# Kernel optimization log

Measured on AMD Instinct MI355X. Metric: run time of the kernel, lower is better.

Reference implementation:

```python
import jax, jax.numpy as jnp
import numpy as np

H = W = 64
ALPHA = 1.0
BETA = 100.0
LIMB_PAIRS = np.array([[0,1],[1,2],[2,3],[0,4],[4,5],[5,6],[0,7],[7,8],[8,9],[9,10],
                       [8,11],[11,12],[12,13],[8,14],[14,15],[15,16]])
P0 = LIMB_PAIRS[:, 0]
P1 = LIMB_PAIRS[:, 1]
_last = {}
for _l, _j in enumerate(P0):
    _last[int(_j)] = _l
J0 = np.array(list(_last.keys()))   # unique proximal joints
L0 = np.array(list(_last.values())) # last limb writing to each joint


def make_kernel(h, w, alpha):
    # replicates: coords = stack(meshgrid(arange(2h-1), arange(2w-1))).transpose(1,2) (h==w)
    ii, jj = jnp.meshgrid(jnp.arange(2 * h - 1), jnp.arange(2 * w - 1), indexing='ij')
    ker = jnp.stack([h - jj, w - ii], axis=0).astype(jnp.float32)  # (2, 2h-1, 2w-1)
    dist = jnp.linalg.norm(ker, axis=0, keepdims=True)
    dist = dist.at[0, h, w].set(1.0)
    return ker / dist ** (1.0 + alpha)


def corr_full(x, k):
    # x: (N, Cin, h, w); k: (Cout, Cin, 2h-1, 2w-1); 'same' correlation with pad h-1/w-1
    h, w = x.shape[-2:]
    return jax.lax.conv_general_dilated(x, k, (1, 1), ((h - 1, h - 1), (w - 1, w - 1)))


def heatmap_std(x, di=False):
    axes = (3, 4, 5) if di else (3, 4)
    return jnp.std(x, axis=axes, keepdims=True, ddof=1)


def heatmap_normalize(x, std, di=False):
    return x * std / (heatmap_std(x, di) + 1e-6)


def l2norm(v, axis):
    return v / jnp.maximum(jnp.linalg.norm(v, axis=axis, keepdims=True), 1e-12)


def soft_argmax(hm, beta):
    # hm: ... x h x w -> ... x 2 with (row_coord, col_coord) as in the torch code
    h, w = hm.shape[-2:]
    p = jax.nn.softmax(hm.reshape(hm.shape[:-2] + (-1,)) * beta, axis=-1).reshape(hm.shape)
    rows = jnp.arange(h, dtype=p.dtype)[:, None]
    cols = jnp.arange(w, dtype=p.dtype)[None, :]
    norm = p.sum((-2, -1))
    kp_x = (p * rows).sum((-2, -1)) / norm
    kp_y = (p * cols).sum((-2, -1)) / norm
    return jnp.stack((kp_x, kp_y), axis=-1)


def scale_pts(pts, image_shape, h, w):
    return jnp.stack((pts[..., 0] * image_shape[1] / w,
                      pts[..., 1] * image_shape[0] / h), axis=-1)


def cofix_forward(heatmaps, fields, Ps, Rs, Cs, image_shape, confs, vth1, vth2, pth1, pth2):
    bs, nv, nL, _, h, w = fields.shape
    nJ = heatmaps.shape[2]
    K = make_kernel(h, w, ALPHA)  # (2, 2h-1, 2w-1)

    heatmaps = heatmaps - jnp.mean(heatmaps, axis=(3, 4), keepdims=True)
    std_hm = heatmap_std(heatmaps, di=False)
    std_df = heatmap_std(fields, di=True)

    Hs = heatmaps[:, :, P1] - heatmaps[:, :, P0]  # (bs, nv, nL, h, w)
    # conv3d(kernel1, flipped Hs) == 'same' correlation of Hs with spatially-reversed K
    k1 = K[:, ::-1, ::-1][:, None]  # (2, 1, 2h-1, 2w-1)
    convs = corr_full(Hs.reshape(-1, 1, h, w), k1).reshape(bs, nv, nL, 2, h, w)

    coef = jax.nn.relu(jnp.sum(convs * fields[..., :2, :, :], axis=3, keepdims=True))
    fields_new = fields * coef

    fnorm = jnp.linalg.norm(fields, axis=3, keepdims=True)
    lvecs = l2norm(jnp.sum(fnorm * fields, axis=(4, 5)), axis=3)
    lpts = scale_pts(soft_argmax(fnorm[:, :, :, 0], BETA), image_shape, h, w)

    fnorm_new = jnp.linalg.norm(fields_new, axis=3, keepdims=True)
    lvecs_new = l2norm(jnp.sum(fnorm_new * fields_new, axis=(4, 5)), axis=3)
    lpts_new = scale_pts(soft_argmax(fnorm_new[:, :, :, 0], BETA), image_shape, h, w)

    # original code computes vec_selection(...) then overwrites: delta[:] = 0
    delta = jnp.zeros((bs, nv, nL, 1), dtype=heatmaps.dtype)
    comb_v = delta * lvecs_new + (1 - delta) * lvecs
    comb_p = delta * lpts_new + (1 - delta) * lpts

    d6 = delta[..., None, None]
    fields_c = heatmap_normalize(fields * (1 - d6) + fields_new * d6, std_df, di=True)

    # conv2d(kernel2, fields) then output spatial flip == 'same' correlation with K
    k2 = K[None]  # (1, 2, 2h-1, 2w-1)
    fds2jts = corr_full(fields_c[..., :2, :, :].reshape(-1, 2, h, w), k2)
    fds2jts = fds2jts.reshape(bs, nv, nL, h, w)
    prox_ = jax.nn.relu(-fds2jts)
    dist_ = jax.nn.relu(fds2jts)

    hms_new = heatmaps.at[:, :, J0].set(heatmaps[:, :, J0] * prox_[:, :, L0])
    hms_new = hms_new.at[:, :, P1].set(hms_new[:, :, P1] * dist_)
    hms_new = heatmap_normalize(hms_new, std_hm, di=False)

    kps = scale_pts(soft_argmax(heatmaps, BETA), image_shape, h, w)[..., None]
    kps_new = scale_pts(soft_argmax(hms_new, BETA), image_shape, h, w)[..., None]
    kps_new = jnp.where(jnp.isnan(kps_new), kps, kps_new)

    # sed_selection (reconstructed): keep refined kps where joint conf is high and
    # the refinement displacement is small.
    confs_j = confs[:, :, nL:]
    disp = jnp.linalg.norm((kps_new - kps)[..., 0], axis=-1)  # (bs, nv, nJ)
    sel = ((confs_j > pth1) & (disp < pth2)).astype(kps.dtype)[..., None, None]
    kps_combined = sel * kps_new + (1 - sel) * kps

    return kps_combined, comb_v, comb_p, fields_new, hms_new


def setup_inputs() -> dict:
    key = jax.random.key(0)
    ks = jax.random.split(key, 6)
    bs, nv, nJ, nL = 4, 4, 17, 16
    return {
        'heatmaps': jax.random.uniform(ks[0], (bs, nv, nJ, H, W), jnp.float32),
        'fields': jax.random.normal(ks[1], (bs, nv, nL, 3, H, W), jnp.float32),
        'Ps': jax.random.normal(ks[2], (bs, nv, 3, 4), jnp.float32),
        'Rs': jax.random.normal(ks[3], (bs, nv, 3, 3), jnp.float32),
        'Cs': jax.random.normal(ks[4], (bs, nv, 3, 1), jnp.float32),
        'image_shape': jnp.array([384, 384], jnp.int32),
        'confs': jax.random.uniform(ks[5], (bs, nv, nL + nJ), jnp.float32),
        'vth1': 0.5, 'vth2': 0.5, 'pth1': 0.1, 'pth2': 20.0,
    }


def reference(heatmaps, fields, Ps, Rs, Cs, image_shape, confs, vth1, vth2, pth1, pth2):
    return cofix_forward(heatmaps, fields, Ps, Rs, Cs, image_shape, confs,
                         vth1, vth2, pth1, pth2)
```

## Files before the change

kernel.cpp:

```cpp
#include <hip/hip_runtime.h>
#include <math.h>

#define TPB 1024
#define HTPB 256
#define NPIX 4096
#define NJ 17
#define NL 16
static constexpr float kBeta = 100.0f;
static constexpr float S2H = 0.70710678118654752f;

#define O_KPS 0
#define O_CV 544
#define O_CP 1312
#define O_FN 1824
#define O_HM 3147552
#define W_FDS 0
#define W_W1 1049376
#define W_W2 1082144

__device__ __constant__ int c_P0[16] = {0,1,2,0,4,5,0,7,8,9,8,11,12,8,14,15};
__device__ __constant__ int c_P1[16] = {1,2,3,4,5,6,7,8,9,10,11,12,13,14,15,16};
__device__ __constant__ int c_proxL[17] = {6,1,2,-1,4,5,-1,7,13,9,-1,11,12,-1,14,15,-1};
__device__ __constant__ int c_distL[17] = {-1,0,1,2,3,4,5,6,7,8,9,10,11,12,13,14,15};

using cplx = float2;
__device__ inline cplx cadd(cplx a, cplx b){ return {a.x+b.x, a.y+b.y}; }
__device__ inline cplx csub(cplx a, cplx b){ return {a.x-b.x, a.y-b.y}; }
__device__ inline cplx cmul(cplx a, cplx w){ return {a.x*w.x - a.y*w.y, a.x*w.y + a.y*w.x}; }
__device__ inline cplx cmulc(cplx a, cplx w){ return {a.x*w.x + a.y*w.y, a.y*w.x - a.x*w.y}; }

__device__ inline void wsync(){
  asm volatile("s_waitcnt lgkmcnt(0)" ::: "memory");
}

__device__ __constant__ float2 W128BR[8] = {
  {1.f,0.f},
  {0.98078528040323044913f,-0.19509032201612826785f},
  {0.99518472667219688624f,-0.09801714032956060199f},
  {0.95694033573220886494f,-0.29028467725446236764f},
  {0.99879545620517239271f,-0.04906767432741801425f},
  {0.97003125319454399260f,-0.24298017990326388995f},
  {0.98917650996478097345f,-0.14673047445536175166f},
  {0.94154406518302077841f,-0.33688985339222005069f}
};
__device__ __constant__ float2 W16BR[8] = {
  {1.f,0.f},
  {0.f,-1.f},
  {0.70710678118654752440f,-0.70710678118654752440f},
  {-0.70710678118654752440f,-0.70710678118654752440f},
  {0.92387953251128675613f,-0.38268343236508977173f},
  {-0.38268343236508977173f,-0.92387953251128675613f},
  {0.38268343236508977173f,-0.92387953251128675613f},
  {-0.92387953251128675613f,-0.38268343236508977173f}
};

__device__ inline void bf8_tail(cplx t0, cplx t1, cplx t2, cplx t3,
                                cplx t4, cplx t5, cplx t6, cplx t7, cplx x[8]){
  cplx u0=cadd(t0,t2), u2=csub(t0,t2);
  cplx u1=cadd(t1,t3), d13=csub(t1,t3);
  cplx u3={d13.y,-d13.x};
  cplx u4=cadd(t4,t6), u6=csub(t4,t6);
  cplx u5=cadd(t5,t7), d57=csub(t5,t7);
  cplx u7={d57.y,-d57.x};
  x[0]=cadd(u0,u1); x[1]=csub(u0,u1);
  x[2]=cadd(u2,u3); x[3]=csub(u2,u3);
  x[4]=cadd(u4,u5); x[5]=csub(u4,u5);
  x[6]=cadd(u6,u7); x[7]=csub(u6,u7);
}
__device__ inline void bf8_fwd(cplx x[8]){
  cplx t0=cadd(x[0],x[4]), d4=csub(x[0],x[4]);
  cplx t1=cadd(x[1],x[5]), d5=csub(x[1],x[5]);
  cplx t2=cadd(x[2],x[6]), d6=csub(x[2],x[6]);
  cplx t3=cadd(x[3],x[7]), d7=csub(x[3],x[7]);
  cplx t5={S2H*(d5.x+d5.y), S2H*(d5.y-d5.x)};
  cplx t6={d6.y,-d6.x};
  cplx t7={S2H*(d7.y-d7.x), -S2H*(d7.x+d7.y)};
  bf8_tail(t0,t1,t2,t3,d4,t5,t6,t7,x);
}
__device__ inline void bf8_fwd_z(cplx x[8]){
  cplx t5={S2H*(x[1].x+x[1].y), S2H*(x[1].y-x[1].x)};
  cplx t6={x[2].y,-x[2].x};
  cplx t7={S2H*(x[3].y-x[3].x), -S2H*(x[3].x+x[3].y)};
  bf8_tail(x[0],x[1],x[2],x[3],x[0],t5,t6,t7,x);
}
__device__ inline void bf8_inv(cplx y[8]){
  cplx u0=cadd(y[0],y[1]), u1=csub(y[0],y[1]);
  cplx u2=cadd(y[2],y[3]), u3=csub(y[2],y[3]);
  cplx u4=cadd(y[4],y[5]), u5=csub(y[4],y[5]);
  cplx u6=cadd(y[6],y[7]), u7=csub(y[6],y[7]);
  cplx t0=cadd(u0,u2), t2=csub(u0,u2);
  cplx iu3={-u3.y,u3.x};
  cplx t1=cadd(u1,iu3), t3=csub(u1,iu3);
  cplx t4=cadd(u4,u6), t6=csub(u4,u6);
  cplx iu7={-u7.y,u7.x};
  cplx t5=cadd(u5,iu7), t7=csub(u5,iu7);
  y[0]=cadd(t0,t4); y[4]=csub(t0,t4);
  cplx w5={S2H*(t5.x-t5.y), S2H*(t5.x+t5.y)};
  y[1]=cadd(t1,w5); y[5]=csub(t1,w5);
  cplx w6={-t6.y,t6.x};
  y[2]=cadd(t2,w6); y[6]=csub(t2,w6);
  cplx w7={-S2H*(t7.x+t7.y), S2H*(t7.x-t7.y)};
  y[3]=cadd(t3,w7); y[7]=csub(t3,w7);
}

__device__ inline void fft16_fwd(cplx z[16]){
  cplx e[8], o[8];
  #pragma unroll
  for (int t=0;t<8;t++){ e[t]=z[2*t]; o[t]=z[2*t+1]; }
  bf8_fwd(e); bf8_fwd(o);
  #pragma unroll
  for (int p=0;p<8;p++){
    cplx vo = cmul(o[p], W16BR[p]);
    z[2*p]   = cadd(e[p], vo);
    z[2*p+1] = csub(e[p], vo);
  }
}
__device__ inline void fft16_inv(cplx z[16]){
  cplx e[8], o[8];
  #pragma unroll
  for (int p=0;p<8;p++){
    cplx a=z[2*p], b=z[2*p+1];
    e[p] = cadd(a,b);
    o[p] = cmulc(csub(a,b), W16BR[p]);
  }
  bf8_inv(e); bf8_inv(o);
  #pragma unroll
  for (int t=0;t<8;t++){ z[2*t]=e[t]; z[2*t+1]=o[t]; }
}

__device__ inline void twchainA(const cplx* TW, int j, cplx A[8]){
  cplx W1 = TW[j];
  cplx W2 = cmul(W1,W1);
  cplx W4 = cmul(W2,W2);
  cplx W6 = cmul(W4,W2);
  A[0] = {1.f,0.f}; A[1] = W4; A[2] = W2; A[3] = W6;
  A[4] = W1; A[5] = cmul(W4,W1); A[6] = cmul(W2,W1); A[7] = cmul(W6,W1);
}

__device__ inline int PH(int y, int m){
  return (y<<6) | ((m ^ ((y&7)*9) ^ ((y>>3)&7)) & 63);
}

template<bool ZT>
__device__ inline void row_s1_f(float4* S4, const cplx* TW, int L, int m){
  cplx xe[8], xo[8];
  #pragma unroll
  for (int t=0; t<(ZT?4:8); t++){
    float4 v = S4[PH(L, m+8*t)];
    xe[t]={v.x,v.y}; xo[t]={v.z,v.w};
  }
  if (ZT){ bf8_fwd_z(xe); bf8_fwd_z(xo); } else { bf8_fwd(xe); bf8_fwd(xo); }
  cplx A[8]; twchainA(TW, 2*m, A);
  #pragma unroll
  for (int p=0;p<8;p++){
    cplx B = cmul(A[p], W128BR[p]);
    cplx ve = cmul(xe[p], A[p]);
    cplx vo = cmul(xo[p], B);
    S4[PH(L, m+8*p)] = {ve.x, ve.y, vo.x, vo.y};
  }
}
__device__ inline void row_s1_i(float4* S4, const cplx* TW, int L, int m){
  cplx xe[8], xo[8];
  #pragma unroll
  for (int p=0;p<8;p++){
    float4 v = S4[PH(L, m+8*p)];
    xe[p]={v.x,v.y}; xo[p]={v.z,v.w};
  }
  cplx A[8]; twchainA(TW, 2*m, A);
  #pragma unroll
  for (int p=0;p<8;p++){
    cplx B = cmul(A[p], W128BR[p]);
    xe[p] = cmulc(xe[p], A[p]);
    xo[p] = cmulc(xo[p], B);
  }
  bf8_inv(xe); bf8_inv(xo);
  #pragma unroll
  for (int t=0;t<4;t++)
    S4[PH(L, m+8*t)] = {xe[t].x, xe[t].y, xo[t].x, xo[t].y};
}
__device__ inline void row_s2_f(float4* S4, int L, int jb){
  cplx z[16];
  #pragma unroll
  for (int k=0;k<8;k++){
    float4 v = S4[PH(L, jb*8+k)];
    z[2*k]={v.x,v.y}; z[2*k+1]={v.z,v.w};
  }
  fft16_fwd(z);
  #pragma unroll
  for (int k=0;k<8;k++)
    S4[PH(L, jb*8+k)] = {z[2*k].x, z[2*k].y, z[2*k+1].x, z[2*k+1].y};
}
__device__ inline void row_s2_i(float4* S4, int L, int jb){
  cplx z[16];
  #pragma unroll
  for (int k=0;k<8;k++){
    float4 v = S4[PH(L, jb*8+k)];
    z[2*k]={v.x,v.y}; z[2*k+1]={v.z,v.w};
  }
  fft16_inv(z);
  #pragma unroll
  for (int k=0;k<8;k++)
    S4[PH(L, jb*8+k)] = {z[2*k].x, z[2*k].y, z[2*k+1].x, z[2*k+1].y};
}
template<bool ZT>
__device__ inline void col_s1_f(float4* S4, const cplx* TW, int yj, int sc){
  cplx xe[8], xo[8];
  #pragma unroll
  for (int t=0; t<(ZT?4:8); t++){
    float4 v = S4[PH(yj+16*t, sc)];
    xe[t]={v.x,v.y}; xo[t]={v.z,v.w};
  }
  if (ZT){ bf8_fwd_z(xe); bf8_fwd_z(xo); } else { bf8_fwd(xe); bf8_fwd(xo); }
  cplx A[8]; twchainA(TW, yj, A);
  #pragma unroll
  for (int p=0;p<8;p++){
    cplx ve = cmul(xe[p], A[p]);
    cplx vo = cmul(xo[p], A[p]);
    S4[PH(yj+16*p, sc)] = {ve.x, ve.y, vo.x, vo.y};
  }
}
__device__ inline void col_s1_i(float4* S4, const cplx* TW, int yj, int sc){
  cplx xe[8], xo[8];
  #pragma unroll
  for (int p=0;p<8;p++){
    float4 v = S4[PH(yj+16*p, sc)];
    xe[p]={v.x,v.y}; xo[p]={v.z,v.w};
  }
  cplx A[8]; twchainA(TW, yj, A);
  #pragma unroll
  for (int p=0;p<8;p++){
    xe[p] = cmulc(xe[p], A[p]);
    xo[p] = cmulc(xo[p], A[p]);
  }
  bf8_inv(xe); bf8_inv(xo);
  #pragma unroll
  for (int t=0;t<4;t++)
    S4[PH(yj+16*t, sc)] = {xe[t].x, xe[t].y, xo[t].x, xo[t].y};
}

__device__ inline float wred(float v){
  #pragma unroll
  for (int o=32;o;o>>=1) v += __shfl_xor(v, o, 64);
  return v;
}
__device__ inline float wredmax(float v){
  #pragma unroll
  for (int o=32;o;o>>=1) v = fmaxf(v, __shfl_xor(v, o, 64));
  return v;
}
template<int NW>
__device__ inline float bred1(float v, float* s0, int tid){
  v = wred(v);
  const int w = tid >> 6;
  if ((tid & 63) == 0) s0[w] = v;
  __syncthreads();
  if (tid == 0){
    float A = 0.f;
    #pragma unroll
    for (int i=0;i<NW;i++) A += s0[i];
    s0[0] = A;
  }
  __syncthreads();
  const float r = s0[0];
  __syncthreads();
  return r;
}
template<int NW>
__device__ inline void bred3(float& a, float& b, float& c,
                             float* s0, float* s1, float* s2, int tid){
  a = wred(a); b = wred(b); c = wred(c);
  const int w = tid >> 6;
  if ((tid & 63) == 0){ s0[w]=a; s1[w]=b; s2[w]=c; }
  __syncthreads();
  if (tid == 0){
    float A=0.f, B=0.f, C=0.f;
    #pragma unroll
    for (int i=0;i<NW;i++){ A+=s0[i]; B+=s1[i]; C+=s2[i]; }
    s0[0]=A; s1[0]=B; s2[0]=C;
  }
  __syncthreads();
  a = s0[0]; b = s1[0]; c = s2[0];
  __syncthreads();
}
template<int NW>
__device__ inline float bredmax(float v, float* s0, int tid){
  v = wredmax(v);
  const int w = tid >> 6;
  if ((tid & 63) == 0) s0[w] = v;
  __syncthreads();
  if (tid == 0){
    float M = s0[0];
    #pragma unroll
    for (int i=1;i<NW;i++) M = fmaxf(M, s0[i]);
    s0[0] = M;
  }
  __syncthreads();
  const float r = s0[0];
  __syncthreads();
  return r;
}

__device__ inline cplx wval(int r, int c, int which){
  const int dy = (r<64)? r : r-128;
  const int dx = (c<64)? c : c-128;
  float a, b;
  if (which==0){ a = 1.f-(float)dy; b = 1.f-(float)dx; }
  else         { a = 1.f+(float)dy; b = 1.f+(float)dx; }
  const float den = a*a + b*b;
  if (r==64 || c==64 || den<=0.f) return {0.f,0.f};
  const float inv = 1.f/den;
  return {a*inv, -b*inv};
}

__global__ __launch_bounds__(TPB,4) void prep_kernel(float* __restrict__ W1,
                                                     float* __restrict__ W2){
  __shared__ float4 S4[8192];
  __shared__ cplx TW[128];
  const int tid = threadIdx.x;
  const int wvx = tid >> 6, lane = tid & 63;
  const int which = blockIdx.x;
  if (tid < 128){
    float s, c;
    sincosf(-6.283185307179586f * (float)tid / 128.0f, &s, &c);
    TW[tid] = {c, s};
  }
  for (int s = tid; s < 8192; s += TPB){
    const int y = s>>6, m = s&63;
    const cplx v0 = wval(y, 2*m, which);
    const cplx v1 = wval(y, 2*m+1, which);
    S4[PH(y, m)] = {v0.x, v0.y, v1.x, v1.y};
  }
  __syncthreads();
  {
    const int L = 8*wvx + (lane>>3), m = lane&7;
    row_s1_f<false>(S4, TW, L, m);
    wsync();
    row_s2_f(S4, L, m);
  }
  __syncthreads();
  {
    const int yj = lane & 15, sc = 4*wvx + (lane>>4);
    col_s1_f<false>(S4, TW, yj, sc);
    wsync();
    cplx* Sc = (cplx*)S4;
    const int c = 8*wvx + (lane&7), r = lane>>3;
    cplx z[16];
    #pragma unroll
    for (int i=0;i<16;i++)
      z[i] = Sc[2*PH(16*r+i, c>>1) + (c&1)];
    fft16_fwd(z);
    cplx* Wo = (cplx*)((which==0)?W1:W2);
    const float scl = 1.0f / 16384.0f;
    #pragma unroll
    for (int i=0;i<16;i++) Wo[(16*r+i)*128 + c] = {z[i].x*scl, z[i].y*scl};
  }
}

__global__ __launch_bounds__(TPB,4) void conv_kernel(const float* __restrict__ heat,
                                                     const float* __restrict__ fields,
                                                     const float* __restrict__ W1g,
                                                     const float* __restrict__ W2g,
                                                     const int* __restrict__ ishape,
                                                     float* __restrict__ out,
                                                     float* __restrict__ fds){
  __shared__ float4 S4[8192];
  __shared__ cplx TW[128];
  __shared__ float sA[16], sB[16], sC[16];
  const int tid = threadIdx.x;
  const int wv = tid >> 6, lane = tid & 63;
  const int n = blockIdx.x;
  const bool is2 = (n < 256);
  const int m_img = is2 ? n : (n - 256);
  if (tid < 128){
    float s, c;
    sincosf(-6.283185307179586f * (float)tid / 128.0f, &s, &c);
    TW[tid] = {c, s};
  }
  const float* f = fields + (size_t)m_img * 3 * NPIX;
  const int y = tid >> 4, x4 = (tid & 15) << 2;
  const int i = (y << 6) + x4;
  const int m = (tid & 15) << 1;
  float sf_loc = 0.0f;
  if (!is2){
    const int bv = m_img >> 4, l = m_img & 15;
    const int j1 = bv*NJ + c_P1[l], j0 = bv*NJ + c_P0[l];
    const float4 a = *(const float4*)(heat + (size_t)j1*NPIX + i);
    const float4 b = *(const float4*)(heat + (size_t)j0*NPIX + i);
    const float d0=a.x-b.x, d1=a.y-b.y, d2=a.z-b.z, d3=a.w-b.w;
    const float dm = bred1<16>(d0+d1+d2+d3, sA, tid) * (1.0f/4096.0f);
    S4[PH(y, m  )] = {d0-dm, 0.f, d1-dm, 0.f};
    S4[PH(y, m+1)] = {d2-dm, 0.f, d3-dm, 0.f};
  } else {
    const float4 A = *(const float4*)(f + NPIX + i);
    const float4 B = *(const float4*)(f + i);
    const float4 C = *(const float4*)(f + 2*NPIX + i);
    S4[PH(y, m  )] = {A.x, B.x, A.y, B.y};
    S4[PH(y, m+1)] = {A.z, B.z, A.w, B.w};
    float s1 = A.x+A.y+A.z+A.w + B.x+B.y+B.z+B.w + C.x+C.y+C.z+C.w;
    float s2 = A.x*A.x+A.y*A.y+A.z*A.z+A.w*A.w
             + B.x*B.x+B.y*B.y+B.z*B.z+B.w*B.w
             + C.x*C.x+C.y*C.y+C.z*C.z+C.w*C.w;
    float d = 0.0f;
    bred3<16>(s1, s2, d, sA, sB, sC, tid);
    const float var = (s2 - s1*s1/12288.0f) / 12287.0f;
    const float sd = sqrtf(fmaxf(var, 0.0f));
    sf_loc = sd / (sd + 1e-6f);
  }
  __syncthreads();
  if (wv < 8){
    const int L = 8*wv + (lane>>3), mm = lane&7;
    row_s1_f<true>(S4, TW, L, mm);
    wsync();
    row_s2_f(S4, L, mm);
  }
  __syncthreads();
  {
    const cplx* Wg = (const cplx*)(is2 ? W2g : W1g);
    const int c = 8*wv + (lane&7), r = lane>>3;
    cplx wvv[16];
    #pragma unroll
    for (int k=0;k<16;k++) wvv[k] = Wg[(16*r+k)*128 + c];
    const int yj = lane & 15, sc = 4*wv + (lane>>4);
    col_s1_f<true>(S4, TW, yj, sc);
    wsync();
    {
      cplx* Sc = (cplx*)S4;
      cplx z[16];
      int ad[16];
      #pragma unroll
      for (int k=0;k<16;k++){
        ad[k] = 2*PH(16*r+k, c>>1) + (c&1);
        z[k] = Sc[ad[k]];
      }
      fft16_fwd(z);
      #pragma unroll
      for (int k=0;k<16;k++) z[k] = cmul(z[k], wvv[k]);
      fft16_inv(z);
      #pragma unroll
      for (int k=0;k<16;k++) Sc[ad[k]] = z[k];
    }
    wsync();
    col_s1_i(S4, TW, yj, sc);
  }
  __syncthreads();
  if (wv < 8){
    const int L = 8*wv + (lane>>3), mm = lane&7;
    row_s2_i(S4, L, mm);
    wsync();
    row_s1_i(S4, TW, L, mm);
  }
  __syncthreads();
  const float4 va = S4[PH(y, m)];
  const float4 vb = S4[PH(y, m+1)];
  if (!is2){
    float* o = out + O_FN + (size_t)m_img * 3 * NPIX;
    const float4 f0 = *(const float4*)(f + i);
    const float4 f1 = *(const float4*)(f + NPIX + i);
    const float4 f2 = *(const float4*)(f + 2*NPIX + i);
    const float c0[4] = {-va.y, -va.w, -vb.y, -vb.w};
    const float c1[4] = { va.x,  va.z,  vb.x,  vb.z};
    const float f0a[4] = {f0.x,f0.y,f0.z,f0.w};
    const float f1a[4] = {f1.x,f1.y,f1.z,f1.w};
    const float f2a[4] = {f2.x,f2.y,f2.z,f2.w};
    float o0[4], o1[4], o2[4], fn[4];
    float a0 = 0.f, a1 = 0.f, a2 = 0.f;
    #pragma unroll
    for (int j=0;j<4;j++){
      const float cf = fmaxf(0.f, c0[j]*f0a[j] + c1[j]*f1a[j]);
      o0[j] = f0a[j]*cf; o1[j] = f1a[j]*cf; o2[j] = f2a[j]*cf;
      const float nn = sqrtf(f0a[j]*f0a[j] + f1a[j]*f1a[j] + f2a[j]*f2a[j]);
      fn[j] = nn;
      a0 += nn*f0a[j]; a1 += nn*f1a[j]; a2 += nn*f2a[j];
    }
    *(float4*)(o + i)          = {o0[0],o0[1],o0[2],o0[3]};
    *(float4*)(o + NPIX + i)   = {o1[0],o1[1],o1[2],o1[3]};
    *(float4*)(o + 2*NPIX + i) = {o2[0],o2[1],o2[2],o2[3]};
    bred3<16>(a0, a1, a2, sA, sB, sC, tid);
    float mx = fmaxf(fmaxf(fn[0],fn[1]), fmaxf(fn[2],fn[3]));
    mx = bredmax<16>(mx, sA, tid);
    float Sm = 0.f, Sx = 0.f, Sy = 0.f;
    #pragma unroll
    for (int j=0;j<4;j++){
      const float e = expf(kBeta * (fn[j] - mx));
      Sm += e; Sx += e * (float)y; Sy += e * (float)(x4 + j);
    }
    bred3<16>(Sm, Sx, Sy, sA, sB, sC, tid);
    if (tid == 0){
      float nrm = sqrtf(a0*a0 + a1*a1 + a2*a2);
      nrm = fmaxf(nrm, 1e-12f);
      out[O_CV + m_img*3 + 0] = a0/nrm;
      out[O_CV + m_img*3 + 1] = a1/nrm;
      out[O_CV + m_img*3 + 2] = a2/nrm;
      const float sxs = (float)ishape[1] / 64.0f;
      const float sys = (float)ishape[0] / 64.0f;
      out[O_CP + m_img*2 + 0] = Sx/Sm * sxs;
      out[O_CP + m_img*2 + 1] = Sy/Sm * sys;
    }
  } else {
    float* o = fds + (size_t)m_img * NPIX;
    *(float4*)(o + i) = {va.x*sf_loc, va.z*sf_loc, vb.x*sf_loc, vb.z*sf_loc};
  }
}

__global__ __launch_bounds__(HTPB) void hms_kernel(const float* __restrict__ heat,
                                                   const float* __restrict__ fds,
                                                   const float* __restrict__ confs,
                                                   const int* __restrict__ ishape,
                                                   const float* __restrict__ pth1p,
                                                   const float* __restrict__ pth2p,
                                                   float* __restrict__ out){
  __shared__ float sA[4], sB[4], sC[4];
  const int tid = threadIdx.x;
  const int idx = blockIdx.x;
  const int bv = idx / NJ, j = idx % NJ;
  const float4* hp4 = (const float4*)(heat + (size_t)idx * NPIX);
  const int pl = c_proxL[j], dl = c_distL[j];
  const float4* fp4 = (pl >= 0) ? (const float4*)(fds + (size_t)(bv*NL + pl) * NPIX) : nullptr;
  const float4* fd4 = (dl >= 0) ? (const float4*)(fds + (size_t)(bv*NL + dl) * NPIX) : nullptr;
  float ho[16], prod[16];
  float s = 0.0f, s2 = 0.0f, dummy = 0.0f;
  #pragma unroll
  for (int i = 0; i < 4; i++){
    const int u = tid + i*HTPB;
    const float4 h4 = hp4[u];
    const float hv[4] = {h4.x, h4.y, h4.z, h4.w};
    float pv[4] = {1.f,1.f,1.f,1.f};
    if (pl >= 0){
      const float4 p4 = fp4[u];
      pv[0] = fmaxf(0.f,-p4.x); pv[1] = fmaxf(0.f,-p4.y);
      pv[2] = fmaxf(0.f,-p4.z); pv[3] = fmaxf(0.f,-p4.w);
    }
    float dv[4] = {1.f,1.f,1.f,1.f};
    if (dl >= 0){
      const float4 d4 = fd4[u];
      dv[0] = fmaxf(0.f,d4.x); dv[1] = fmaxf(0.f,d4.y);
      dv[2] = fmaxf(0.f,d4.z); dv[3] = fmaxf(0.f,d4.w);
    }
    #pragma unroll
    for (int k=0;k<4;k++){
      ho[4*i+k] = hv[k];
      prod[4*i+k] = pv[k]*dv[k];
      s += hv[k]; s2 += hv[k]*hv[k];
    }
  }
  bred3<4>(s, s2, dummy, sA, sB, sC, tid);
  const float mh = s / 4096.0f;
  const float sdh = sqrtf(fmaxf((s2 - s*mh) / 4095.0f, 0.0f));
  float hn[16];
  float sn = 0.0f, sn2 = 0.0f; dummy = 0.0f;
  #pragma unroll
  for (int i = 0; i < 16; i++){
    ho[i] -= mh;
    const float mm = ho[i]*prod[i];
    hn[i] = mm;
    sn += mm; sn2 += mm*mm;
  }
  bred3<4>(sn, sn2, dummy, sA, sB, sC, tid);
  const float varn = (sn2 - sn*sn/4096.0f) / 4095.0f;
  const float sdn = sqrtf(fmaxf(varn, 0.0f));
  const float scale = sdh / (sdn + 1e-6f);
  float4* ohm4 = (float4*)(out + O_HM + (size_t)idx * NPIX);
  #pragma unroll
  for (int i = 0; i < 4; i++){
    #pragma unroll
    for (int k=0;k<4;k++) hn[4*i+k] *= scale;
    ohm4[tid + i*HTPB] = {hn[4*i], hn[4*i+1], hn[4*i+2], hn[4*i+3]};
  }
  float mo = -1e30f, mn = -1e30f;
  #pragma unroll
  for (int i = 0; i < 16; i++){ mo = fmaxf(mo, ho[i]); mn = fmaxf(mn, hn[i]); }
  mo = bredmax<4>(mo, sA, tid);
  mn = bredmax<4>(mn, sA, tid);
  float So = 0.0f, Sxo = 0.0f, Syo = 0.0f;
  float Sn = 0.0f, Sxn = 0.0f, Syn = 0.0f;
  #pragma unroll
  for (int i = 0; i < 16; i++){
    const int px = (tid + (i>>2)*HTPB)*4 + (i&3);
    const float yy = (float)(px >> 6), xx = (float)(px & 63);
    const float eo = expf(kBeta * (ho[i] - mo));
    So += eo; Sxo += eo*yy; Syo += eo*xx;
    const float en = expf(kBeta * (hn[i] - mn));
    Sn += en; Sxn += en*yy; Syn += en*xx;
  }
  bred3<4>(So, Sxo, Syo, sA, sB, sC, tid);
  bred3<4>(Sn, Sxn, Syn, sA, sB, sC, tid);
  if (tid == 0){
    const float sxs = (float)ishape[1] / 64.0f;
    const float sys = (float)ishape[0] / 64.0f;
    const float kxo = Sxo/So * sxs, kyo = Syo/So * sys;
    float kxn = Sxn/Sn * sxs, kyn = Syn/Sn * sys;
    if (kxn != kxn) kxn = kxo;
    if (kyn != kyn) kyn = kyo;
    const float ddx = kxn - kxo, ddy = kyn - kyo;
    const float disp = sqrtf(ddx*ddx + ddy*ddy);
    const float conf = confs[bv*(NL+NJ) + NL + j];
    const bool sel = (conf > pth1p[0]) && (disp < pth2p[0]);
    out[O_KPS + idx*2 + 0] = sel ? kxn : kxo;
    out[O_KPS + idx*2 + 1] = sel ? kyn : kyo;
  }
}

extern "C" void kernel_launch(void* const* d_in, const int* in_sizes, int n_in,
                              void* d_out, int out_size, void* d_ws, size_t ws_size,
                              hipStream_t stream) {
  const float* heat   = (const float*)d_in[0];
  const float* fields = (const float*)d_in[1];
  const int*   ishape = (const int*)d_in[5];
  const float* confs  = (const float*)d_in[6];
  const float* pth1   = (const float*)d_in[9];
  const float* pth2   = (const float*)d_in[10];
  float* out = (float*)d_out;
  float* ws = (float*)d_ws;
  float* fds = ws + W_FDS;
  float* W1  = ws + W_W1;
  float* W2  = ws + W_W2;

  hipLaunchKernelGGL(prep_kernel, dim3(2), dim3(TPB), 0, stream, W1, W2);
  hipLaunchKernelGGL(conv_kernel, dim3(512), dim3(TPB), 0, stream,
                     heat, fields, W1, W2, ishape, out, fds);
  hipLaunchKernelGGL(hms_kernel, dim3(272), dim3(HTPB), 0, stream,
                     heat, fds, confs, ishape, pth1, pth2, out);
}
```

Measured before the change: 147.8 us.

## Cut block-reduction barriers and retune LDS swizzle and row-stage thread mapping

Replaces the three-barrier block reduction helpers with single-barrier reductions where every thread sums the per-wave partials from shared memory. Related reductions are merged into packed float2/float4 slots, e.g. the max is folded into the sum reduction. It also adds another XOR term to the LDS swizzle and swaps the lane-to-row mapping in the second row FFT stage to reduce bank conflicts. The cost is more shared-memory reads per thread and distinct reduction buffers to avoid reuse hazards.

```diff
diff --git a/kernel.cpp b/kernel.cpp
--- a/kernel.cpp
+++ b/kernel.cpp
@@ -138,7 +138,7 @@
 }
 
 __device__ inline int PH(int y, int m){
-  return (y<<6) | ((m ^ ((y&7)*9) ^ ((y>>3)&7)) & 63);
+  return (y<<6) | ((m ^ ((y&7)*9) ^ ((y>>3)&7) ^ (((y>>4)&1)<<2)) & 63);
 }
 
 template<bool ZT>
@@ -247,57 +247,6 @@
   #pragma unroll
   for (int o=32;o;o>>=1) v = fmaxf(v, __shfl_xor(v, o, 64));
   return v;
-}
-template<int NW>
-__device__ inline float bred1(float v, float* s0, int tid){
-  v = wred(v);
-  const int w = tid >> 6;
-  if ((tid & 63) == 0) s0[w] = v;
-  __syncthreads();
-  if (tid == 0){
-    float A = 0.f;
-    #pragma unroll
-    for (int i=0;i<NW;i++) A += s0[i];
-    s0[0] = A;
-  }
-  __syncthreads();
-  const float r = s0[0];
-  __syncthreads();
-  return r;
-}
-template<int NW>
-__device__ inline void bred3(float& a, float& b, float& c,
-                             float* s0, float* s1, float* s2, int tid){
-  a = wred(a); b = wred(b); c = wred(c);
-  const int w = tid >> 6;
-  if ((tid & 63) == 0){ s0[w]=a; s1[w]=b; s2[w]=c; }
-  __syncthreads();
-  if (tid == 0){
-    float A=0.f, B=0.f, C=0.f;
-    #pragma unroll
-    for (int i=0;i<NW;i++){ A+=s0[i]; B+=s1[i]; C+=s2[i]; }
-    s0[0]=A; s1[0]=B; s2[0]=C;
-  }
-  __syncthreads();
-  a = s0[0]; b = s1[0]; c = s2[0];
-  __syncthreads();
-}
-template<int NW>
-__device__ inline float bredmax(float v, float* s0, int tid){
-  v = wredmax(v);
-  const int w = tid >> 6;
-  if ((tid & 63) == 0) s0[w] = v;
-  __syncthreads();
-  if (tid == 0){
-    float M = s0[0];
-    #pragma unroll
-    for (int i=1;i<NW;i++) M = fmaxf(M, s0[i]);
-    s0[0] = M;
-  }
-  __syncthreads();
-  const float r = s0[0];
-  __syncthreads();
-  return r;
 }
 
 __device__ inline cplx wval(int r, int c, int which){
@@ -332,10 +281,9 @@
   }
   __syncthreads();
   {
-    const int L = 8*wvx + (lane>>3), m = lane&7;
-    row_s1_f<false>(S4, TW, L, m);
+    row_s1_f<false>(S4, TW, 8*wvx + (lane>>3), lane&7);
     wsync();
-    row_s2_f(S4, L, m);
+    row_s2_f(S4, 8*wvx + (lane&7), lane>>3);
   }
   __syncthreads();
   {
@@ -365,7 +313,8 @@
                                                      float* __restrict__ fds){
   __shared__ float4 S4[8192];
   __shared__ cplx TW[128];
-  __shared__ float sA[16], sB[16], sC[16];
+  __shared__ float2 R2A[16];
+  __shared__ float4 R4A[16], R4B[16];
   const int tid = threadIdx.x;
   const int wv = tid >> 6, lane = tid & 63;
   const int n = blockIdx.x;
@@ -387,7 +336,13 @@
     const float4 a = *(const float4*)(heat + (size_t)j1*NPIX + i);
     const float4 b = *(const float4*)(heat + (size_t)j0*NPIX + i);
     const float d0=a.x-b.x, d1=a.y-b.y, d2=a.z-b.z, d3=a.w-b.w;
-    const float dm = bred1<16>(d0+d1+d2+d3, sA, tid) * (1.0f/4096.0f);
+    const float ps = wred(d0+d1+d2+d3);
+    if (lane == 0) R2A[wv].x = ps;
+    __syncthreads();
+    float S = 0.f;
+    #pragma unroll
+    for (int k2=0;k2<16;k2++) S += R2A[k2].x;
+    const float dm = S * (1.0f/4096.0f);
     S4[PH(y, m  )] = {d0-dm, 0.f, d1-dm, 0.f};
     S4[PH(y, m+1)] = {d2-dm, 0.f, d3-dm, 0.f};
   } else {
@@ -400,18 +355,21 @@
     float s2 = A.x*A.x+A.y*A.y+A.z*A.z+A.w*A.w
              + B.x*B.x+B.y*B.y+B.z*B.z+B.w*B.w
              + C.x*C.x+C.y*C.y+C.z*C.z+C.w*C.w;
-    float d = 0.0f;
-    bred3<16>(s1, s2, d, sA, sB, sC, tid);
-    const float var = (s2 - s1*s1/12288.0f) / 12287.0f;
+    const float2 pr = {wred(s1), wred(s2)};
+    if (lane == 0) R2A[wv] = pr;
+    __syncthreads();
+    float S1 = 0.f, S2 = 0.f;
+    #pragma unroll
+    for (int k2=0;k2<16;k2++){ S1 += R2A[k2].x; S2 += R2A[k2].y; }
+    const float var = (S2 - S1*S1/12288.0f) / 12287.0f;
     const float sd = sqrtf(fmaxf(var, 0.0f));
     sf_loc = sd / (sd + 1e-6f);
   }
   __syncthreads();
   if (wv < 8){
-    const int L = 8*wv + (lane>>3), mm = lane&7;
-    row_s1_f<true>(S4, TW, L, mm);
+    row_s1_f<true>(S4, TW, 8*wv + (lane>>3), lane&7);
     wsync();
-    row_s2_f(S4, L, mm);
+    row_s2_f(S4, 8*wv + (lane&7), lane>>3);
   }
   __syncthreads();
   {
@@ -444,10 +402,9 @@
   }
   __syncthreads();
   if (wv < 8){
-    const int L = 8*wv + (lane>>3), mm = lane&7;
-    row_s2_i(S4, L, mm);
+    row_s2_i(S4, 8*wv + (lane&7), lane>>3);
     wsync();
-    row_s1_i(S4, TW, L, mm);
+    row_s1_i(S4, TW, 8*wv + (lane>>3), lane&7);
   }
   __syncthreads();
   const float4 va = S4[PH(y, m)];
@@ -475,26 +432,41 @@
     *(float4*)(o + i)          = {o0[0],o0[1],o0[2],o0[3]};
     *(float4*)(o + NPIX + i)   = {o1[0],o1[1],o1[2],o1[3]};
     *(float4*)(o + 2*NPIX + i) = {o2[0],o2[1],o2[2],o2[3]};
-    bred3<16>(a0, a1, a2, sA, sB, sC, tid);
     float mx = fmaxf(fmaxf(fn[0],fn[1]), fmaxf(fn[2],fn[3]));
-    mx = bredmax<16>(mx, sA, tid);
+    const float4 p1 = {wred(a0), wred(a1), wred(a2), wredmax(mx)};
+    if (lane == 0) R4A[wv] = p1;
+    __syncthreads();
+    float A0=0.f, A1=0.f, A2=0.f, MX=-1e30f;
+    #pragma unroll
+    for (int k2=0;k2<16;k2++){
+      const float4 q = R4A[k2];
+      A0 += q.x; A1 += q.y; A2 += q.z; MX = fmaxf(MX, q.w);
+    }
     float Sm = 0.f, Sx = 0.f, Sy = 0.f;
     #pragma unroll
     for (int j=0;j<4;j++){
-      const float e = expf(kBeta * (fn[j] - mx));
+      const float e = expf(kBeta * (fn[j] - MX));
       Sm += e; Sx += e * (float)y; Sy += e * (float)(x4 + j);
     }
-    bred3<16>(Sm, Sx, Sy, sA, sB, sC, tid);
+    const float4 p2 = {wred(Sm), wred(Sx), wred(Sy), 0.f};
+    if (lane == 0) R4B[wv] = p2;
+    __syncthreads();
     if (tid == 0){
-      float nrm = sqrtf(a0*a0 + a1*a1 + a2*a2);
+      float SM=0.f, SX=0.f, SY=0.f;
+      #pragma unroll
+      for (int k2=0;k2<16;k2++){
+        const float4 q = R4B[k2];
+        SM += q.x; SX += q.y; SY += q.z;
+      }
+      float nrm = sqrtf(A0*A0 + A1*A1 + A2*A2);
       nrm = fmaxf(nrm, 1e-12f);
-      out[O_CV + m_img*3 + 0] = a0/nrm;
-      out[O_CV + m_img*3 + 1] = a1/nrm;
-      out[O_CV + m_img*3 + 2] = a2/nrm;
+      out[O_CV + m_img*3 + 0] = A0/nrm;
+      out[O_CV + m_img*3 + 1] = A1/nrm;
+      out[O_CV + m_img*3 + 2] = A2/nrm;
       const float sxs = (float)ishape[1] / 64.0f;
       const float sys = (float)ishape[0] / 64.0f;
-      out[O_CP + m_img*2 + 0] = Sx/Sm * sxs;
-      out[O_CP + m_img*2 + 1] = Sy/Sm * sys;
+      out[O_CP + m_img*2 + 0] = SX/SM * sxs;
+      out[O_CP + m_img*2 + 1] = SY/SM * sys;
     }
   } else {
     float* o = fds + (size_t)m_img * NPIX;
@@ -509,8 +481,10 @@
                                                    const float* __restrict__ pth1p,
                                                    const float* __restrict__ pth2p,
                                                    float* __restrict__ out){
-  __shared__ float sA[4], sB[4], sC[4];
+  __shared__ float2 H2A[4], H2B[4], H2C[4];
+  __shared__ float4 H4A[4], H4B[4];
   const int tid = threadIdx.x;
+  const int wv = tid >> 6, lane = tid & 63;
   const int idx = blockIdx.x;
   const int bv = idx / NJ, j = idx % NJ;
   const float4* hp4 = (const float4*)(heat + (size_t)idx * NPIX);
@@ -518,7 +492,7 @@
   const float4* fp4 = (pl >= 0) ? (const float4*)(fds + (size_t)(bv*NL + pl) * NPIX) : nullptr;
   const float4* fd4 = (dl >= 0) ? (const float4*)(fds + (size_t)(bv*NL + dl) * NPIX) : nullptr;
   float ho[16], prod[16];
-  float s = 0.0f, s2 = 0.0f, dummy = 0.0f;
+  float s = 0.0f, s2 = 0.0f;
   #pragma unroll
   for (int i = 0; i < 4; i++){
     const int u = tid + i*HTPB;
@@ -543,11 +517,18 @@
       s += hv[k]; s2 += hv[k]*hv[k];
     }
   }
-  bred3<4>(s, s2, dummy, sA, sB, sC, tid);
-  const float mh = s / 4096.0f;
-  const float sdh = sqrtf(fmaxf((s2 - s*mh) / 4095.0f, 0.0f));
+  {
+    const float2 p = {wred(s), wred(s2)};
+    if (lane == 0) H2A[wv] = p;
+  }
+  __syncthreads();
+  float S = 0.f, S2 = 0.f;
+  #pragma unroll
+  for (int k=0;k<4;k++){ S += H2A[k].x; S2 += H2A[k].y; }
+  const float mh = S / 4096.0f;
+  const float sdh = sqrtf(fmaxf((S2 - S*mh) / 4095.0f, 0.0f));
   float hn[16];
-  float sn = 0.0f, sn2 = 0.0f; dummy = 0.0f;
+  float sn = 0.0f, sn2 = 0.0f;
   #pragma unroll
   for (int i = 0; i < 16; i++){
     ho[i] -= mh;
@@ -555,8 +536,15 @@
     hn[i] = mm;
     sn += mm; sn2 += mm*mm;
   }
-  bred3<4>(sn, sn2, dummy, sA, sB, sC, tid);
-  const float varn = (sn2 - sn*sn/4096.0f) / 4095.0f;
+  {
+    const float2 p = {wred(sn), wred(sn2)};
+    if (lane == 0) H2B[wv] = p;
+  }
+  __syncthreads();
+  float SN = 0.f, SN2 = 0.f;
+  #pragma unroll
+  for (int k=0;k<4;k++){ SN += H2B[k].x; SN2 += H2B[k].y; }
+  const float varn = (SN2 - SN*SN/4096.0f) / 4095.0f;
   const float sdn = sqrtf(fmaxf(varn, 0.0f));
   const float scale = sdh / (sdn + 1e-6f);
   float4* ohm4 = (float4*)(out + O_HM + (size_t)idx * NPIX);
@@ -569,26 +557,43 @@
   float mo = -1e30f, mn = -1e30f;
   #pragma unroll
   for (int i = 0; i < 16; i++){ mo = fmaxf(mo, ho[i]); mn = fmaxf(mn, hn[i]); }
-  mo = bredmax<4>(mo, sA, tid);
-  mn = bredmax<4>(mn, sA, tid);
+  {
+    const float2 p = {wredmax(mo), wredmax(mn)};
+    if (lane == 0) H2C[wv] = p;
+  }
+  __syncthreads();
+  float MO = -1e30f, MN = -1e30f;
+  #pragma unroll
+  for (int k=0;k<4;k++){ MO = fmaxf(MO, H2C[k].x); MN = fmaxf(MN, H2C[k].y); }
   float So = 0.0f, Sxo = 0.0f, Syo = 0.0f;
   float Sn = 0.0f, Sxn = 0.0f, Syn = 0.0f;
   #pragma unroll
   for (int i = 0; i < 16; i++){
     const int px = (tid + (i>>2)*HTPB)*4 + (i&3);
     const float yy = (float)(px >> 6), xx = (float)(px & 63);
-    const float eo = expf(kBeta * (ho[i] - mo));
+    const float eo = expf(kBeta * (ho[i] - MO));
     So += eo; Sxo += eo*yy; Syo += eo*xx;
-    const float en = expf(kBeta * (hn[i] - mn));
+    const float en = expf(kBeta * (hn[i] - MN));
     Sn += en; Sxn += en*yy; Syn += en*xx;
   }
-  bred3<4>(So, Sxo, Syo, sA, sB, sC, tid);
-  bred3<4>(Sn, Sxn, Syn, sA, sB, sC, tid);
+  {
+    const float4 pa = {wred(So), wred(Sxo), wred(Syo), 0.f};
+    const float4 pb = {wred(Sn), wred(Sxn), wred(Syn), 0.f};
+    if (lane == 0){ H4A[wv] = pa; H4B[wv] = pb; }
+  }
+  __syncthreads();
   if (tid == 0){
+    float SO=0.f, SXO=0.f, SYO=0.f, SNN=0.f, SXN=0.f, SYN=0.f;
+    #pragma unroll
+    for (int k=0;k<4;k++){
+      const float4 qa = H4A[k], qb = H4B[k];
+      SO += qa.x; SXO += qa.y; SYO += qa.z;
+      SNN += qb.x; SXN += qb.y; SYN += qb.z;
+    }
     const float sxs = (float)ishape[1] / 64.0f;
     const float sys = (float)ishape[0] / 64.0f;
-    const float kxo = Sxo/So * sxs, kyo = Syo/So * sys;
-    float kxn = Sxn/Sn * sxs, kyn = Syn/Sn * sys;
+    const float kxo = SXO/SO * sxs, kyo = SYO/SO * sys;
+    float kxn = SXN/SNN * sxs, kyn = SYN/SNN * sys;
     if (kxn != kxn) kxn = kxo;
     if (kyn != kyn) kyn = kyo;
     const float ddx = kxn - kxo, ddy = kyn - kyo;
```

Measured after the change: 140.9 us. -4.6%, faster.
